# Optimization experiments

Measured on AMD Instinct MI355X. Metric: run time of the kernel, lower is better.

## Reference

```python
import jax, jax.numpy as jnp
import numpy as np


def setup_inputs() -> dict:
    key = jax.random.key(0)
    k1, k2, k3 = jax.random.split(key, 3)
    N, E, D_IN, D_OUT = 100000, 3200000, 256, 256
    x = jax.random.normal(k1, (N, D_IN), dtype=jnp.float32)
    W = jax.random.normal(k2, (D_OUT, D_IN), dtype=jnp.float32) * (1.0 / np.sqrt(D_IN))
    edge_index = jax.random.randint(k3, (2, E), 0, N, dtype=jnp.int32)
    return {"x": x, "W": W, "edge_index": edge_index}


def reference(x, W, edge_index):
    N = x.shape[0]
    # add self loops (static shape: E + N edges)
    loops = jnp.arange(N, dtype=edge_index.dtype)
    src = jnp.concatenate([edge_index[0], loops])  # [E+N]
    dst = jnp.concatenate([edge_index[1], loops])  # [E+N]
    # symmetric degree normalization: deg = bincount over source index
    deg = jax.ops.segment_sum(jnp.ones_like(src, dtype=x.dtype), src, num_segments=N)
    deg_rsqrt = jax.lax.rsqrt(deg)
    vals = deg_rsqrt[src] * deg_rsqrt[dst]  # [E+N]
    # dense projection then SpMM: out[i] = sum_e A[src_e=i] * h[dst_e]
    h = x @ W.T  # [N, D_OUT]
    msgs = vals[:, None] * h[dst]  # gather + scale
    out = jax.ops.segment_sum(msgs, src, num_segments=N)  # scatter-add
    return out
```

## Files before the change

### kernel.cpp

```cpp
#include <hip/hip_runtime.h>
#include <hip/hip_bf16.h>
#include <stdint.h>

#define D 256
#define NBUCK 391
#define BSHIFT 8
#define TILE 4096

typedef short short8 __attribute__((ext_vector_type(8)));
typedef float f32x4 __attribute__((ext_vector_type(4)));

__device__ __forceinline__ float bf2f(unsigned short u) {
  return __uint_as_float(((unsigned)u) << 16);
}
__device__ __forceinline__ unsigned short f2bf(float f) {
  unsigned u = __float_as_uint(f);
  unsigned r = u + 0x7FFFu + ((u >> 16) & 1u);
  return (unsigned short)(r >> 16);
}

__global__ void bucket_hist_kernel(const int* __restrict__ src, int* __restrict__ bcount, int E) {
  __shared__ int h[NBUCK];
  for (int i = threadIdx.x; i < NBUCK; i += 256) h[i] = 0;
  __syncthreads();
  int gid = blockIdx.x * 256 + threadIdx.x;
  for (int e = gid; e < E; e += 256 * 256) atomicAdd(&h[src[e] >> BSHIFT], 1);
  __syncthreads();
  for (int i = threadIdx.x; i < NBUCK; i += 256) {
    int c = h[i];
    if (c) atomicAdd(&bcount[i], c);
  }
}

__global__ void bucket_scan_kernel(const int* __restrict__ bcount, int* __restrict__ bbase,
                                   int* __restrict__ gcursor) {
  __shared__ int sc[2][512];
  int tid = threadIdx.x;
  sc[0][tid] = (tid < NBUCK) ? bcount[tid] : 0;
  __syncthreads();
  int d = 0;
  for (int off = 1; off < 512; off <<= 1) {
    int v = sc[d][tid];
    if (tid >= off) v += sc[d][tid - off];
    sc[d ^ 1][tid] = v;
    __syncthreads();
    d ^= 1;
  }
  if (tid < NBUCK) {
    int excl = (tid == 0) ? 0 : sc[d][tid - 1];
    bbase[tid] = excl;
    gcursor[tid] = excl;
  }
}

__launch_bounds__(256)
__global__ void binscatter_kernel(const int* __restrict__ src, const int* __restrict__ dst,
                                  int* __restrict__ gcursor, int* __restrict__ ebuf, int E) {
  __shared__ int hist[NBUCK];
  __shared__ int lstart[512];
  __shared__ int gbase[NBUCK];
  __shared__ int sc[2][512];
  __shared__ int stag[TILE];
  __shared__ unsigned short sbuck[TILE];

  int tid = threadIdx.x;
  int base = blockIdx.x * TILE;
  int tilecount = E - base;
  if (tilecount > TILE) tilecount = TILE;

  for (int i = tid; i < NBUCK; i += 256) hist[i] = 0;
  __syncthreads();

  int esrc[16], edst[16];
#pragma unroll
  for (int k = 0; k < 16; k++) {
    int e = base + k * 256 + tid;
    if (e < E) {
      esrc[k] = src[e];
      edst[k] = dst[e];
      atomicAdd(&hist[esrc[k] >> BSHIFT], 1);
    } else {
      esrc[k] = -1;
      edst[k] = 0;
    }
  }
  __syncthreads();

  for (int i = tid; i < 512; i += 256) sc[0][i] = (i < NBUCK) ? hist[i] : 0;
  __syncthreads();
  int d = 0;
  for (int off = 1; off < 512; off <<= 1) {
    for (int i = tid; i < 512; i += 256) {
      int v = sc[d][i];
      if (i >= off) v += sc[d][i - off];
      sc[d ^ 1][i] = v;
    }
    __syncthreads();
    d ^= 1;
  }
  for (int i = tid; i < 512; i += 256) lstart[i] = (i == 0) ? 0 : sc[d][i - 1];
  __syncthreads();

  for (int b = tid; b < NBUCK; b += 256) {
    int c = hist[b];
    if (c) gbase[b] = atomicAdd(&gcursor[b], c);
  }
  __syncthreads();

  for (int i = tid; i < NBUCK; i += 256) hist[i] = 0;
  __syncthreads();

#pragma unroll
  for (int k = 0; k < 16; k++) {
    if (esrc[k] >= 0) {
      int b = esrc[k] >> BSHIFT;
      int r = atomicAdd(&hist[b], 1);
      int pos = lstart[b] + r;
      stag[pos] = edst[k] | ((esrc[k] & 255) << 20);
      sbuck[pos] = (unsigned short)b;
    }
  }
  __syncthreads();

  for (int s = tid; s < tilecount; s += 256) {
    int b = sbuck[s];
    ebuf[gbase[b] + (s - lstart[b])] = stag[s];
  }
}

__launch_bounds__(256)
__global__ void bucketsort_kernel(const int* __restrict__ ebuf, const int* __restrict__ bbase,
                                  const int* __restrict__ bcount, int* __restrict__ csr,
                                  int* __restrict__ offsets, int* __restrict__ ecount,
                                  float* __restrict__ rnorm, int N) {
  __shared__ int ncnt[256];
  __shared__ int nstart[256];
  __shared__ int sc[2][256];
  int tid = threadIdx.x;
  int b = blockIdx.x;
  int base = bbase[b];
  int cnt = bcount[b];
  int node0 = b << BSHIFT;

  ncnt[tid] = 0;
  __syncthreads();
  for (int s = tid; s < cnt; s += 256) {
    int v = ebuf[base + s];
    atomicAdd(&ncnt[v >> 20], 1);
  }
  __syncthreads();

  int mycnt = ncnt[tid];
  sc[0][tid] = mycnt;
  __syncthreads();
  int d = 0;
  for (int off = 1; off < 256; off <<= 1) {
    int v = sc[d][tid];
    if (tid >= off) v += sc[d][tid - off];
    sc[d ^ 1][tid] = v;
    __syncthreads();
    d ^= 1;
  }
  nstart[tid] = (tid == 0) ? 0 : sc[d][tid - 1];
  __syncthreads();

  int node = node0 + tid;
  if (node < N) {
    offsets[node] = base + nstart[tid];
    ecount[node] = mycnt;
    rnorm[node] = rsqrtf((float)(mycnt + 1));
  }

  ncnt[tid] = 0;
  __syncthreads();
  for (int s = tid; s < cnt; s += 256) {
    int v = ebuf[base + s];
    int nl = v >> 20;
    int r = atomicAdd(&ncnt[nl], 1);
    csr[base + nstart[nl] + r] = v & 0xFFFFF;
  }
}

__global__ void convx_kernel(const float* __restrict__ x, unsigned short* __restrict__ xb,
                             int n, int npad) {
  int i4 = blockIdx.x * 256 + threadIdx.x;
  long long elem = (long long)i4 * 4;
  if (elem >= (long long)npad * D) return;
  int row = (int)(elem / D);
  ushort4 o;
  if (row < n) {
    const float4 v = *(const float4*)&x[elem];
    o.x = f2bf(v.x); o.y = f2bf(v.y); o.z = f2bf(v.z); o.w = f2bf(v.w);
  } else {
    o = make_ushort4(0, 0, 0, 0);
  }
  *(ushort4*)&xb[elem] = o;
}

__global__ void convw_kernel(const float* __restrict__ w, unsigned short* __restrict__ wb) {
  int i4 = blockIdx.x * 256 + threadIdx.x;
  int elem = i4 * 4;
  const float4 v = *(const float4*)&w[elem];
  ushort4 o;
  o.x = f2bf(v.x); o.y = f2bf(v.y); o.z = f2bf(v.z); o.w = f2bf(v.w);
  *(ushort4*)&wb[elem] = o;
}

__launch_bounds__(256)
__global__ void gemm_kernel(const unsigned short* __restrict__ A,
                            const unsigned short* __restrict__ B,
                            unsigned short* __restrict__ Hout,
                            const float* __restrict__ rnorm, int n) {
  __shared__ unsigned short sA[128 * 32];
  __shared__ unsigned short sB[128 * 32];
  int tid = threadIdx.x;
  int wave = tid >> 6, lane = tid & 63;
  int wm = wave >> 1, wn = wave & 1;
  int l16 = lane & 15, quad = lane >> 4;
  int arow0 = blockIdx.x * 128;
  int brow0 = blockIdx.y * 128;

  f32x4 acc[4][4];
  const f32x4 zero = {0.f, 0.f, 0.f, 0.f};
#pragma unroll
  for (int i = 0; i < 4; i++)
#pragma unroll
    for (int j = 0; j < 4; j++) acc[i][j] = zero;

  for (int k0 = 0; k0 < 256; k0 += 32) {
#pragma unroll
    for (int it = 0; it < 2; ++it) {
      int c = it * 256 + tid;
      int row = c >> 2, cc = (c & 3) * 8;
      *(int4*)&sA[c * 8] = *(const int4*)&A[(arow0 + row) * 256 + k0 + cc];
      *(int4*)&sB[c * 8] = *(const int4*)&B[(brow0 + row) * 256 + k0 + cc];
    }
    __syncthreads();
    short8 af[4], bfr[4];
#pragma unroll
    for (int i = 0; i < 4; i++)
      af[i] = *(const short8*)&sA[(wm * 64 + i * 16 + l16) * 32 + quad * 8];
#pragma unroll
    for (int j = 0; j < 4; j++)
      bfr[j] = *(const short8*)&sB[(wn * 64 + j * 16 + l16) * 32 + quad * 8];
#pragma unroll
    for (int i = 0; i < 4; i++)
#pragma unroll
      for (int j = 0; j < 4; j++)
        acc[i][j] = __builtin_amdgcn_mfma_f32_16x16x32_bf16(af[i], bfr[j], acc[i][j], 0, 0, 0);
    __syncthreads();
  }

#pragma unroll
  for (int i = 0; i < 4; i++) {
    int rowb = arow0 + wm * 64 + i * 16 + quad * 4;
#pragma unroll
    for (int r = 0; r < 4; r++) {
      int gr = rowb + r;
      float rn = (gr < n) ? rnorm[gr] : 0.f;
#pragma unroll
      for (int j = 0; j < 4; j++) {
        int col = brow0 + wn * 64 + j * 16 + l16;
        Hout[gr * 256 + col] = f2bf(acc[i][j][r] * rn);
      }
    }
  }
}

__launch_bounds__(256)
__global__ void gather_kernel(const unsigned short* __restrict__ hs,
                              const int* __restrict__ offsets,
                              const int* __restrict__ ecount,
                              const float* __restrict__ rnorm,
                              const int* __restrict__ csr,
                              float* __restrict__ out, int n) {
  int wave = threadIdx.x >> 6, lane = threadIdx.x & 63;
  int node = blockIdx.x * 4 + wave;
  if (node >= n) return;
  int start = offsets[node], cnt = ecount[node];
  float a0 = 0.f, a1 = 0.f, a2 = 0.f, a3 = 0.f;
  for (int base = 0; base < cnt; base += 64) {
    int m = cnt - base;
    if (m > 64) m = 64;
    int idxv = 0;
    if (lane < m) idxv = csr[start + base + lane];
    int t = 0;
    for (; t + 4 <= m; t += 4) {
      int d0 = __shfl(idxv, t);
      int d1 = __shfl(idxv, t + 1);
      int d2 = __shfl(idxv, t + 2);
      int d3 = __shfl(idxv, t + 3);
      ushort4 u0 = *(const ushort4*)&hs[d0 * 256 + lane * 4];
      ushort4 u1 = *(const ushort4*)&hs[d1 * 256 + lane * 4];
      ushort4 u2 = *(const ushort4*)&hs[d2 * 256 + lane * 4];
      ushort4 u3 = *(const ushort4*)&hs[d3 * 256 + lane * 4];
      a0 += bf2f(u0.x) + bf2f(u1.x) + bf2f(u2.x) + bf2f(u3.x);
      a1 += bf2f(u0.y) + bf2f(u1.y) + bf2f(u2.y) + bf2f(u3.y);
      a2 += bf2f(u0.z) + bf2f(u1.z) + bf2f(u2.z) + bf2f(u3.z);
      a3 += bf2f(u0.w) + bf2f(u1.w) + bf2f(u2.w) + bf2f(u3.w);
    }
    for (; t < m; ++t) {
      int dd = __shfl(idxv, t);
      ushort4 u = *(const ushort4*)&hs[dd * 256 + lane * 4];
      a0 += bf2f(u.x); a1 += bf2f(u.y); a2 += bf2f(u.z); a3 += bf2f(u.w);
    }
  }
  ushort4 us = *(const ushort4*)&hs[node * 256 + lane * 4];
  float rn = rnorm[node];
  float4 o;
  o.x = rn * (a0 + bf2f(us.x));
  o.y = rn * (a1 + bf2f(us.y));
  o.z = rn * (a2 + bf2f(us.z));
  o.w = rn * (a3 + bf2f(us.w));
  *(float4*)&out[node * 256 + lane * 4] = o;
}

extern "C" void kernel_launch(void* const* d_in, const int* in_sizes, int n_in,
                              void* d_out, int out_size, void* d_ws, size_t ws_size,
                              hipStream_t stream) {
  const float* x = (const float*)d_in[0];
  const float* W = (const float*)d_in[1];
  const int* ei = (const int*)d_in[2];
  float* out = (float*)d_out;

  int N = in_sizes[0] / D;
  int E = in_sizes[2] / 2;
  int NPAD = (N + 127) & ~127;
  const int* src = ei;
  const int* dst = ei + E;

  char* p = (char*)d_ws;
  auto alloc = [&](size_t b) {
    char* r = p;
    p += (b + 255) & ~(size_t)255;
    return r;
  };
  unsigned short* xb = (unsigned short*)alloc((size_t)NPAD * D * 2);
  unsigned short* wb = (unsigned short*)alloc((size_t)D * D * 2);
  unsigned short* hb = (unsigned short*)alloc((size_t)NPAD * D * 2);
  int* csr = (int*)alloc((size_t)E * 4);
  int* offsets = (int*)alloc((size_t)N * 4);
  int* ecount = (int*)alloc((size_t)N * 4);
  float* rnorm = (float*)alloc((size_t)N * 4);
  int* bcount = (int*)alloc(NBUCK * 4);
  int* bbase = (int*)alloc(NBUCK * 4);
  int* gcursor = (int*)alloc(NBUCK * 4);
  int* ebuf = (int*)hb;

  hipMemsetAsync(bcount, 0, NBUCK * 4, stream);
  bucket_hist_kernel<<<256, 256, 0, stream>>>(src, bcount, E);
  bucket_scan_kernel<<<1, 512, 0, stream>>>(bcount, bbase, gcursor);
  binscatter_kernel<<<(E + TILE - 1) / TILE, 256, 0, stream>>>(src, dst, gcursor, ebuf, E);
  bucketsort_kernel<<<NBUCK, 256, 0, stream>>>(ebuf, bbase, bcount, csr, offsets, ecount, rnorm, N);
  convx_kernel<<<(NPAD * (D / 4) + 255) / 256, 256, 0, stream>>>(x, xb, N, NPAD);
  convw_kernel<<<(D * D / 4) / 256, 256, 0, stream>>>(W, wb);
  gemm_kernel<<<dim3(NPAD / 128, D / 128), 256, 0, stream>>>(xb, wb, hb, rnorm, N);
  gather_kernel<<<(N + 3) / 4, 256, 0, stream>>>(hb, offsets, ecount, rnorm, csr, out, N);
}
```

Before: 539.3 us.

## Split gather into two column-half passes to shrink per-pass working set

The SpMM gather now runs as two launches, each covering 128 of the 256 output columns. Each lane loads 4 bytes instead of 8 per neighbour row, and the unroll doubles to 8 neighbours. The aim is to halve the gathered footprint of the bf16 H matrix per pass (about 25.6MB instead of 51MB) so random row reads hit the L2/MALL cache more often. The cost is reading the CSR indices and offsets twice and issuing narrower 256-byte row segments per wave.

```diff
diff --git a/kernel.cpp b/kernel.cpp
--- a/kernel.cpp
+++ b/kernel.cpp
@@ -273,46 +273,58 @@
                               const int* __restrict__ ecount,
                               const float* __restrict__ rnorm,
                               const int* __restrict__ csr,
-                              float* __restrict__ out, int n) {
+                              float* __restrict__ out, int n, int colbase) {
   int wave = threadIdx.x >> 6, lane = threadIdx.x & 63;
   int node = blockIdx.x * 4 + wave;
   if (node >= n) return;
   int start = offsets[node], cnt = ecount[node];
-  float a0 = 0.f, a1 = 0.f, a2 = 0.f, a3 = 0.f;
+  const unsigned short* hcol = hs + colbase + lane * 2;
+  float a0 = 0.f, a1 = 0.f;
   for (int base = 0; base < cnt; base += 64) {
     int m = cnt - base;
     if (m > 64) m = 64;
     int idxv = 0;
     if (lane < m) idxv = csr[start + base + lane];
     int t = 0;
-    for (; t + 4 <= m; t += 4) {
+    for (; t + 8 <= m; t += 8) {
       int d0 = __shfl(idxv, t);
       int d1 = __shfl(idxv, t + 1);
       int d2 = __shfl(idxv, t + 2);
       int d3 = __shfl(idxv, t + 3);
-      ushort4 u0 = *(const ushort4*)&hs[d0 * 256 + lane * 4];
-      ushort4 u1 = *(const ushort4*)&hs[d1 * 256 + lane * 4];
-      ushort4 u2 = *(const ushort4*)&hs[d2 * 256 + lane * 4];
-      ushort4 u3 = *(const ushort4*)&hs[d3 * 256 + lane * 4];
-      a0 += bf2f(u0.x) + bf2f(u1.x) + bf2f(u2.x) + bf2f(u3.x);
-      a1 += bf2f(u0.y) + bf2f(u1.y) + bf2f(u2.y) + bf2f(u3.y);
-      a2 += bf2f(u0.z) + bf2f(u1.z) + bf2f(u2.z) + bf2f(u3.z);
-      a3 += bf2f(u0.w) + bf2f(u1.w) + bf2f(u2.w) + bf2f(u3.w);
+      int d4 = __shfl(idxv, t + 4);
+      int d5 = __shfl(idxv, t + 5);
+      int d6 = __shfl(idxv, t + 6);
+      int d7 = __shfl(idxv, t + 7);
+      unsigned u0 = *(const unsigned*)&hcol[d0 * 256];
+      unsigned u1 = *(const unsigned*)&hcol[d1 * 256];
+      unsigned u2 = *(const unsigned*)&hcol[d2 * 256];
+      unsigned u3 = *(const unsigned*)&hcol[d3 * 256];
+      unsigned u4 = *(const unsigned*)&hcol[d4 * 256];
+      unsigned u5 = *(const unsigned*)&hcol[d5 * 256];
+      unsigned u6 = *(const unsigned*)&hcol[d6 * 256];
+      unsigned u7 = *(const unsigned*)&hcol[d7 * 256];
+      a0 += bf2f((unsigned short)u0) + bf2f((unsigned short)u1) +
+            bf2f((unsigned short)u2) + bf2f((unsigned short)u3) +
+            bf2f((unsigned short)u4) + bf2f((unsigned short)u5) +
+            bf2f((unsigned short)u6) + bf2f((unsigned short)u7);
+      a1 += bf2f((unsigned short)(u0 >> 16)) + bf2f((unsigned short)(u1 >> 16)) +
+            bf2f((unsigned short)(u2 >> 16)) + bf2f((unsigned short)(u3 >> 16)) +
+            bf2f((unsigned short)(u4 >> 16)) + bf2f((unsigned short)(u5 >> 16)) +
+            bf2f((unsigned short)(u6 >> 16)) + bf2f((unsigned short)(u7 >> 16));
     }
     for (; t < m; ++t) {
       int dd = __shfl(idxv, t);
-      ushort4 u = *(const ushort4*)&hs[dd * 256 + lane * 4];
-      a0 += bf2f(u.x); a1 += bf2f(u.y); a2 += bf2f(u.z); a3 += bf2f(u.w);
-    }
-  }
-  ushort4 us = *(const ushort4*)&hs[node * 256 + lane * 4];
+      unsigned u = *(const unsigned*)&hcol[dd * 256];
+      a0 += bf2f((unsigned short)u);
+      a1 += bf2f((unsigned short)(u >> 16));
+    }
+  }
+  unsigned us = *(const unsigned*)&hcol[node * 256];
   float rn = rnorm[node];
-  float4 o;
-  o.x = rn * (a0 + bf2f(us.x));
-  o.y = rn * (a1 + bf2f(us.y));
-  o.z = rn * (a2 + bf2f(us.z));
-  o.w = rn * (a3 + bf2f(us.w));
-  *(float4*)&out[node * 256 + lane * 4] = o;
+  float2 o;
+  o.x = rn * (a0 + bf2f((unsigned short)us));
+  o.y = rn * (a1 + bf2f((unsigned short)(us >> 16)));
+  *(float2*)&out[node * 256 + colbase + lane * 2] = o;
 }
 
 extern "C" void kernel_launch(void* const* d_in, const int* in_sizes, int n_in,
@@ -355,5 +367,6 @@
   convx_kernel<<<(NPAD * (D / 4) + 255) / 256, 256, 0, stream>>>(x, xb, N, NPAD);
   convw_kernel<<<(D * D / 4) / 256, 256, 0, stream>>>(W, wb);
   gemm_kernel<<<dim3(NPAD / 128, D / 128), 256, 0, stream>>>(xb, wb, hb, rnorm, N);
-  gather_kernel<<<(N + 3) / 4, 256, 0, stream>>>(hb, offsets, ecount, rnorm, csr, out, N);
-}
+  gather_kernel<<<(N + 3) / 4, 256, 0, stream>>>(hb, offsets, ecount, rnorm, csr, out, N, 0);
+  gather_kernel<<<(N + 3) / 4, 256, 0, stream>>>(hb, offsets, ecount, rnorm, csr, out, N, 128);
+}
```

Measured after the change: 528.2 us. -2.0%, faster.
